# Performance work log

Hardware: AMD Instinct MI355X
Metric: run time of the kernel (lower is better)

Reference implementation:

```python
import jax, jax.numpy as jnp
import numpy as np

D_MODEL = 1024
NUM_HEADS = 16
D_K = D_MODEL // NUM_HEADS


def setup_inputs() -> dict:
    key = jax.random.key(0)
    ks = jax.random.split(key, 9)
    s = 1.0 / np.sqrt(D_MODEL)
    x = jax.random.normal(ks[0], (2, 2048, D_MODEL), dtype=jnp.float32)
    Wq = jax.random.uniform(ks[1], (D_MODEL, D_MODEL), jnp.float32, -s, s)
    bq = jax.random.uniform(ks[2], (D_MODEL,), jnp.float32, -s, s)
    Wk = jax.random.uniform(ks[3], (D_MODEL, D_MODEL), jnp.float32, -s, s)
    bk = jax.random.uniform(ks[4], (D_MODEL,), jnp.float32, -s, s)
    Wv = jax.random.uniform(ks[5], (D_MODEL, D_MODEL), jnp.float32, -s, s)
    bv = jax.random.uniform(ks[6], (D_MODEL,), jnp.float32, -s, s)
    Wo = jax.random.uniform(ks[7], (D_MODEL, D_MODEL), jnp.float32, -s, s)
    bo = jax.random.uniform(ks[8], (D_MODEL,), jnp.float32, -s, s)
    return {"x": x, "Wq": Wq, "bq": bq, "Wk": Wk, "bk": bk,
            "Wv": Wv, "bv": bv, "Wo": Wo, "bo": bo}


def reference(x, Wq, bq, Wk, bk, Wv, bv, Wo, bo):
    B, S, _ = x.shape
    # projections (torch Linear: x @ W.T + b; here W stored as [in, out])
    q = (x @ Wq + bq).reshape(B, S, NUM_HEADS, D_K).transpose(0, 2, 1, 3)
    k = (x @ Wk + bk).reshape(B, S, NUM_HEADS, D_K).transpose(0, 2, 1, 3)
    v = (x @ Wv + bv).reshape(B, S, NUM_HEADS, D_K).transpose(0, 2, 1, 3)
    scores = jnp.einsum('bhqd,bhkd->bhqk', q, k) / jnp.sqrt(jnp.float32(D_K))
    attn = jax.nn.softmax(scores, axis=-1)
    out = jnp.einsum('bhqk,bhkd->bhqd', attn, v)  # [B,H,S,Dk]
    out = out.transpose(0, 2, 1, 3).reshape(B, S, D_MODEL)
    return out @ Wo + bo
```

## Files before the change

### kernel.cpp

```cpp
#include <hip/hip_runtime.h>
#include <hip/hip_bf16.h>

#define SEQ   2048
#define DM    1024
#define NH    16
#define DK    64
#define BATCH 2
#define M_TOT 4096
#define C1 0.18033688011112042f

typedef __attribute__((ext_vector_type(8))) short bf16x8;
typedef __attribute__((ext_vector_type(4))) float f32x4;
typedef unsigned short u16;

__device__ inline u16 f2b(float f) {
    union { float f; unsigned u; } x; x.f = f;
    return (u16)((x.u + 0x7FFFu + ((x.u >> 16) & 1u)) >> 16);
}

__device__ inline unsigned pk2(float a, float b) {
    __hip_bfloat162 h = __float22bfloat162_rn(make_float2(a, b));
    return *reinterpret_cast<unsigned*>(&h);
}

__device__ inline void async_cp16(const u16* g, u16* l) {
    __builtin_amdgcn_global_load_lds(
        (const __attribute__((address_space(1))) unsigned int*)g,
        (__attribute__((address_space(3))) unsigned int*)l, 16, 0, 0);
}

__global__ __launch_bounds__(256) void cast_x(
    const float4* __restrict__ x, uint2* __restrict__ xb)
{
    int gid = blockIdx.x * 256 + threadIdx.x;
    float4 v = x[gid];
    uint2 o;
    o.x = pk2(v.x, v.y); o.y = pk2(v.z, v.w);
    xb[gid] = o;
}

__global__ __launch_bounds__(256) void transpose_cast4(
    const float* __restrict__ W0, const float* __restrict__ W1,
    const float* __restrict__ W2, const float* __restrict__ W3,
    u16* __restrict__ WtBase)
{
    __shared__ float tile[32][33];
    const int t = threadIdx.x;
    const int n0 = blockIdx.x << 5, k0 = blockIdx.y << 5, z = blockIdx.z;
    const float* W = (z == 0) ? W0 : (z == 1) ? W1 : (z == 2) ? W2 : W3;
    u16* Wt = WtBase + (size_t)z * DM * DM;
    #pragma unroll
    for (int i = 0; i < 4; ++i) {
        int idx = t + (i << 8); int r = idx >> 5, c = idx & 31;
        tile[r][c] = W[(size_t)(k0 + r) * DM + n0 + c];
    }
    __syncthreads();
    #pragma unroll
    for (int i = 0; i < 4; ++i) {
        int idx = t + (i << 8); int r = idx >> 5, c = idx & 31;
        Wt[(size_t)(n0 + r) * DM + k0 + c] = f2b(tile[c][r]);
    }
}

__global__ __launch_bounds__(256) void gemm_bt(
    const u16* __restrict__ A, const u16* __restrict__ Bt, int mode,
    const float* __restrict__ bias0, const float* __restrict__ bias1,
    const float* __restrict__ bias2,
    void* __restrict__ out0, void* __restrict__ out1, void* __restrict__ out2)
{
    __shared__ u16 sh[128 * 64 * 2];
    u16* As = sh;
    u16* Bs = sh + 128 * 64;
    const int t = threadIdx.x, wid = t >> 6, lane = t & 63;
    const int lr = lane & 15, quad = lane >> 4;
    const int m0 = blockIdx.y << 7, n0 = blockIdx.x << 7;
    const int wm = (wid & 1) << 6, wn = (wid >> 1) << 6;
    const int lrow = lane >> 3;
    const int scol = (((lane & 7) ^ lrow) << 3);
    const int c0 = ((quad ^ (lr & 7)) << 3);
    const int c1 = (((quad + 4) ^ (lr & 7)) << 3);

    f32x4 acc[4][4];
    #pragma unroll
    for (int i = 0; i < 4; ++i)
        #pragma unroll
        for (int j = 0; j < 4; ++j) acc[i][j] = (f32x4){0.f, 0.f, 0.f, 0.f};

    for (int k0 = 0; k0 < DM; k0 += 64) {
        #pragma unroll
        for (int i = 0; i < 4; ++i) {
            int rb = 32 * i + 8 * wid;
            async_cp16(A  + (size_t)(m0 + rb + lrow) * DM + k0 + scol, As + rb * 64);
            async_cp16(Bt + (size_t)(n0 + rb + lrow) * DM + k0 + scol, Bs + rb * 64);
        }
        __syncthreads();
        #pragma unroll
        for (int h = 0; h < 2; ++h) {
            const int cc = h ? c1 : c0;
            bf16x8 af[4], bfr[4];
            #pragma unroll
            for (int mt = 0; mt < 4; ++mt)
                af[mt] = *(const bf16x8*)(As + (wm + 16 * mt + lr) * 64 + cc);
            #pragma unroll
            for (int nt = 0; nt < 4; ++nt)
                bfr[nt] = *(const bf16x8*)(Bs + (wn + 16 * nt + lr) * 64 + cc);
            #pragma unroll
            for (int mt = 0; mt < 4; ++mt)
                #pragma unroll
                for (int nt = 0; nt < 4; ++nt)
                    acc[mt][nt] = __builtin_amdgcn_mfma_f32_16x16x32_bf16(
                        af[mt], bfr[nt], acc[mt][nt], 0, 0, 0);
        }
        __syncthreads();
    }

    if (mode == 1) {
        u16* wstrip = sh + wid * 1152;
        const int ngb = n0 + wn;
        const int which = ngb >> 10, nnb = ngb & 1023;
        const int h = nnb >> 6;
        const float* bp = (which == 0) ? bias0 : (which == 1) ? bias1 : bias2;
        const float sc = (which == 0) ? C1 : 1.0f;
        float bias_v[4];
        #pragma unroll
        for (int nt = 0; nt < 4; ++nt) bias_v[nt] = bp[nnb + 16 * nt + lr];

        if (which != 1) {
            u16* dst = (which == 0) ? (u16*)out0 : (u16*)out2;
            #pragma unroll
            for (int mt = 0; mt < 4; ++mt) {
                #pragma unroll
                for (int nt = 0; nt < 4; ++nt) {
                    uint2 w;
                    w.x = pk2((acc[mt][nt][0] + bias_v[nt]) * sc,
                              (acc[mt][nt][1] + bias_v[nt]) * sc);
                    w.y = pk2((acc[mt][nt][2] + bias_v[nt]) * sc,
                              (acc[mt][nt][3] + bias_v[nt]) * sc);
                    *(uint2*)(wstrip + (16 * nt + lr) * 16 + quad * 4) = w;
                }
                asm volatile("s_waitcnt lgkmcnt(0)" ::: "memory");
                #pragma unroll
                for (int half = 0; half < 2; ++half) {
                    int id = lane + 64 * half;
                    int d = id >> 1, cho = (id & 1) << 3;
                    int m = m0 + wm + 16 * mt + cho;
                    int b = m >> 11, s = m & (SEQ - 1);
                    *(uint4*)(dst + ((size_t)(b * NH + h) * DK + d) * SEQ + s) =
                        *(const uint4*)(wstrip + d * 16 + cho);
                }
                asm volatile("s_waitcnt lgkmcnt(0)" ::: "memory");
            }
        } else {
            u16* dst = (u16*)out1;
            #pragma unroll
            for (int mt = 0; mt < 4; ++mt) {
                #pragma unroll
                for (int nt = 0; nt < 4; ++nt)
                    #pragma unroll
                    for (int r = 0; r < 4; ++r)
                        wstrip[(quad * 4 + r) * 72 + 16 * nt + lr] =
                            f2b(acc[mt][nt][r] + bias_v[nt]);
                asm volatile("s_waitcnt lgkmcnt(0)" ::: "memory");
                #pragma unroll
                for (int half = 0; half < 2; ++half) {
                    int id = lane + 64 * half;
                    int mloc = id >> 3, dl = (id & 7) << 3;
                    int m = m0 + wm + 16 * mt + mloc;
                    int b = m >> 11, s = m & (SEQ - 1);
                    *(uint4*)(dst + ((size_t)(b * NH + h) * SEQ + s) * DK + dl) =
                        *(const uint4*)(wstrip + mloc * 72 + dl);
                }
                asm volatile("s_waitcnt lgkmcnt(0)" ::: "memory");
            }
        }
    } else {
        float* O = (float*)out0;
        #pragma unroll
        for (int nt = 0; nt < 4; ++nt) {
            int ng = n0 + wn + 16 * nt + lr;
            float bv_ = bias0[ng];
            #pragma unroll
            for (int mt = 0; mt < 4; ++mt) {
                int mr = m0 + wm + 16 * mt + (quad << 2);
                f32x4 v = acc[mt][nt];
                O[(size_t)mr * DM + ng]       = v.x + bv_;
                O[(size_t)(mr + 1) * DM + ng] = v.y + bv_;
                O[(size_t)(mr + 2) * DM + ng] = v.z + bv_;
                O[(size_t)(mr + 3) * DM + ng] = v.w + bv_;
            }
        }
    }
}

__global__ __launch_bounds__(256) void attn_mfma(
    const u16* __restrict__ Qt, const u16* __restrict__ K,
    const u16* __restrict__ Vt, u16* __restrict__ A)
{
    __shared__ u16 sh[20480];

    const int t = threadIdx.x, wid = t >> 6, lane = t & 63;
    const int lr = lane & 15, quad = lane >> 4;
    const int bx = blockIdx.x;
    const int xcd = bx & 7, within = bx >> 3;
    const int bh  = xcd * 4 + (within >> 5);
    const int q0  = (within & 31) << 6;

    const u16* Kb = K  + (size_t)bh * SEQ * DK;
    const u16* Vb = Vt + (size_t)bh * DK * SEQ;

    const int q = q0 + 16 * wid + lr;
    const u16* Qb = Qt + (size_t)bh * DK * SEQ + q;
    bf16x8 bQ0, bQ1;
    #pragma unroll
    for (int j = 0; j < 8; ++j) {
        bQ0[j] = (short)Qb[(size_t)(quad * 8 + j) * SEQ];
        bQ1[j] = (short)Qb[(size_t)(32 + quad * 8 + j) * SEQ];
    }

    f32x4 O[4];
    #pragma unroll
    for (int mt = 0; mt < 4; ++mt) O[mt] = (f32x4){0.f, 0.f, 0.f, 0.f};
    float l_r = 0.f;

    const int srow = t >> 3, schunk = t & 7;
    const int sslot = ((schunk ^ (srow & 7)) << 3);
    const int soff0 = srow * 64 + sslot;
    const int soff1 = (srow + 32) * 64 + sslot;
    const int c0 = ((quad ^ (lr & 7)) << 3);
    const int c1 = (((quad + 4) ^ (lr & 7)) << 3);
    const int prow = 16384 + (16 * wid + lr) * 64;

    uint4 kr0 = *(const uint4*)(Kb + (size_t)srow * DK + schunk * 8);
    uint4 kr1 = *(const uint4*)(Kb + (size_t)(srow + 32) * DK + schunk * 8);
    uint4 vr0 = *(const uint4*)(Vb + (size_t)srow * SEQ + schunk * 8);
    uint4 vr1 = *(const uint4*)(Vb + (size_t)(srow + 32) * SEQ + schunk * 8);
    *(uint4*)(sh + soff0) = kr0;
    *(uint4*)(sh + soff1) = kr1;
    *(uint4*)(sh + 8192 + soff0) = vr0;
    *(uint4*)(sh + 8192 + soff1) = vr1;
    kr0 = *(const uint4*)(Kb + (size_t)(64 + srow) * DK + schunk * 8);
    kr1 = *(const uint4*)(Kb + (size_t)(64 + srow + 32) * DK + schunk * 8);
    vr0 = *(const uint4*)(Vb + (size_t)srow * SEQ + 64 + schunk * 8);
    vr1 = *(const uint4*)(Vb + (size_t)(srow + 32) * SEQ + 64 + schunk * 8);
    __syncthreads();

    for (int it = 0; it < SEQ / 64; ++it) {
        const int kbase = (it & 1) << 12;
        const int vbase = 8192 + ((it & 1) << 12);

        f32x4 S[4];
        #pragma unroll
        for (int mt = 0; mt < 4; ++mt) {
            bf16x8 a0 = *(const bf16x8*)(sh + kbase + (16 * mt + lr) * 64 + c0);
            bf16x8 a1 = *(const bf16x8*)(sh + kbase + (16 * mt + lr) * 64 + c1);
            f32x4 s = (f32x4){0.f, 0.f, 0.f, 0.f};
            s = __builtin_amdgcn_mfma_f32_16x16x32_bf16(a0, bQ0, s, 0, 0, 0);
            s = __builtin_amdgcn_mfma_f32_16x16x32_bf16(a1, bQ1, s, 0, 0, 0);
            S[mt] = s;
        }

        #pragma unroll
        for (int mt = 0; mt < 4; ++mt) {
            float e0 = __builtin_amdgcn_exp2f(S[mt][0]);
            float e1 = __builtin_amdgcn_exp2f(S[mt][1]);
            float e2 = __builtin_amdgcn_exp2f(S[mt][2]);
            float e3 = __builtin_amdgcn_exp2f(S[mt][3]);
            l_r += (e0 + e1) + (e2 + e3);
            uint2 pk;
            pk.x = pk2(e0, e1); pk.y = pk2(e2, e3);
            int chunk = 2 * mt + (quad >> 1);
            *(uint2*)(sh + prow + ((chunk ^ (lr & 7)) << 3)
                         + ((quad & 1) << 2)) = pk;
        }
        asm volatile("s_waitcnt lgkmcnt(0)" ::: "memory");

        bf16x8 p0 = *(const bf16x8*)(sh + prow + c0);
        bf16x8 p1 = *(const bf16x8*)(sh + prow + c1);
        #pragma unroll
        for (int mt = 0; mt < 4; ++mt) {
            bf16x8 v0 = *(const bf16x8*)(sh + vbase + (16 * mt + lr) * 64 + c0);
            bf16x8 v1 = *(const bf16x8*)(sh + vbase + (16 * mt + lr) * 64 + c1);
            O[mt] = __builtin_amdgcn_mfma_f32_16x16x32_bf16(v0, p0, O[mt], 0, 0, 0);
            O[mt] = __builtin_amdgcn_mfma_f32_16x16x32_bf16(v1, p1, O[mt], 0, 0, 0);
        }

        if (it < SEQ / 64 - 1) {
            const int kn = ((it + 1) & 1) << 12;
            const int vn = 8192 + (((it + 1) & 1) << 12);
            *(uint4*)(sh + kn + soff0) = kr0;
            *(uint4*)(sh + kn + soff1) = kr1;
            *(uint4*)(sh + vn + soff0) = vr0;
            *(uint4*)(sh + vn + soff1) = vr1;
            if (it < SEQ / 64 - 2) {
                int nt2 = (it + 2) * 64;
                kr0 = *(const uint4*)(Kb + (size_t)(nt2 + srow) * DK + schunk * 8);
                kr1 = *(const uint4*)(Kb + (size_t)(nt2 + srow + 32) * DK + schunk * 8);
                vr0 = *(const uint4*)(Vb + (size_t)srow * SEQ + nt2 + schunk * 8);
                vr1 = *(const uint4*)(Vb + (size_t)(srow + 32) * SEQ + nt2 + schunk * 8);
            }
            __syncthreads();
        }
    }

    l_r += __shfl_xor(l_r, 16);
    l_r += __shfl_xor(l_r, 32);

    const int b = bh >> 4, h = bh & 15;
    float inv = 1.f / l_r;
    #pragma unroll
    for (int mt = 0; mt < 4; ++mt) {
        uint2 pk;
        pk.x = pk2(O[mt][0] * inv, O[mt][1] * inv);
        pk.y = pk2(O[mt][2] * inv, O[mt][3] * inv);
        *(uint2*)(A + (size_t)(b * SEQ + q) * DM + h * DK + 16 * mt + 4 * quad) = pk;
    }
}

extern "C" void kernel_launch(void* const* d_in, const int* in_sizes, int n_in,
                              void* d_out, int out_size, void* d_ws, size_t ws_size,
                              hipStream_t stream)
{
    const float* x  = (const float*)d_in[0];
    const float* Wq = (const float*)d_in[1];
    const float* bq = (const float*)d_in[2];
    const float* Wk = (const float*)d_in[3];
    const float* bk = (const float*)d_in[4];
    const float* Wv = (const float*)d_in[5];
    const float* bv = (const float*)d_in[6];
    const float* Wo = (const float*)d_in[7];
    const float* bo = (const float*)d_in[8];

    const size_t NE = (size_t)M_TOT * DM;
    u16* xb     = (u16*)d_ws;
    u16* wt_qkv = xb + NE;
    u16* wt_o   = wt_qkv + 3 * (size_t)DM * DM;
    u16* qt_ws  = wt_o + (size_t)DM * DM;
    u16* k_ws   = qt_ws + NE;
    u16* vt_ws  = k_ws + NE;
    u16* a_ws   = vt_ws + NE;

    cast_x<<<M_TOT * DM / 4 / 256, 256, 0, stream>>>((const float4*)x, (uint2*)xb);
    transpose_cast4<<<dim3(32, 32, 4), 256, 0, stream>>>(Wq, Wk, Wv, Wo, wt_qkv);

    gemm_bt<<<dim3(24, 32), 256, 0, stream>>>(
        xb, wt_qkv, 1, bq, bk, bv, qt_ws, k_ws, vt_ws);

    attn_mfma<<<dim3(1024), 256, 0, stream>>>(qt_ws, k_ws, vt_ws, a_ws);

    gemm_bt<<<dim3(8, 32), 256, 0, stream>>>(
        a_ws, wt_o, 0, bo, nullptr, nullptr, d_out, nullptr, nullptr);
}
```

Measured before the change: 228.4 us.

## Halve GEMM K-tile to 32 with new LDS swizzle and stage output stores through LDS

The bf16 GEMM main loop now uses a K step of 32 instead of 64, with a rotated LDS swizzle sized to the smaller tile. This cuts shared memory per block, which may allow more resident blocks, but doubles the number of barriers and loop iterations. The fp32 output-projection epilogue now writes accumulators into a padded LDS strip per wave and then stores coalesced float4 rows, replacing scattered scalar global stores.

```diff
diff --git a/kernel.cpp b/kernel.cpp
--- a/kernel.cpp
+++ b/kernel.cpp
@@ -68,17 +68,16 @@
     const float* __restrict__ bias2,
     void* __restrict__ out0, void* __restrict__ out1, void* __restrict__ out2)
 {
-    __shared__ u16 sh[128 * 64 * 2];
+    __shared__ u16 sh[9216];
     u16* As = sh;
-    u16* Bs = sh + 128 * 64;
+    u16* Bs = sh + 4096;
     const int t = threadIdx.x, wid = t >> 6, lane = t & 63;
     const int lr = lane & 15, quad = lane >> 4;
     const int m0 = blockIdx.y << 7, n0 = blockIdx.x << 7;
     const int wm = (wid & 1) << 6, wn = (wid >> 1) << 6;
-    const int lrow = lane >> 3;
-    const int scol = (((lane & 7) ^ lrow) << 3);
-    const int c0 = ((quad ^ (lr & 7)) << 3);
-    const int c1 = (((quad + 4) ^ (lr & 7)) << 3);
+    const int rowA = lane >> 2;
+    const int colA = (((lane & 3) - ((lane >> 3) & 3)) & 3) << 3;
+    const int sA = (((lr >> 1) + quad) & 3) << 3;
 
     f32x4 acc[4][4];
     #pragma unroll
@@ -86,31 +85,29 @@
         #pragma unroll
         for (int j = 0; j < 4; ++j) acc[i][j] = (f32x4){0.f, 0.f, 0.f, 0.f};
 
-    for (int k0 = 0; k0 < DM; k0 += 64) {
-        #pragma unroll
-        for (int i = 0; i < 4; ++i) {
-            int rb = 32 * i + 8 * wid;
-            async_cp16(A  + (size_t)(m0 + rb + lrow) * DM + k0 + scol, As + rb * 64);
-            async_cp16(Bt + (size_t)(n0 + rb + lrow) * DM + k0 + scol, Bs + rb * 64);
+    for (int k0 = 0; k0 < DM; k0 += 32) {
+        #pragma unroll
+        for (int i = 0; i < 2; ++i) {
+            int ch = wid * 2 + i;
+            async_cp16(A  + (size_t)(m0 + ch * 16 + rowA) * DM + k0 + colA,
+                       As + ch * 16 * 32);
+            async_cp16(Bt + (size_t)(n0 + ch * 16 + rowA) * DM + k0 + colA,
+                       Bs + ch * 16 * 32);
         }
         __syncthreads();
-        #pragma unroll
-        for (int h = 0; h < 2; ++h) {
-            const int cc = h ? c1 : c0;
-            bf16x8 af[4], bfr[4];
-            #pragma unroll
-            for (int mt = 0; mt < 4; ++mt)
-                af[mt] = *(const bf16x8*)(As + (wm + 16 * mt + lr) * 64 + cc);
+        bf16x8 af[4], bfr[4];
+        #pragma unroll
+        for (int mt = 0; mt < 4; ++mt)
+            af[mt] = *(const bf16x8*)(As + (wm + 16 * mt + lr) * 32 + sA);
+        #pragma unroll
+        for (int nt = 0; nt < 4; ++nt)
+            bfr[nt] = *(const bf16x8*)(Bs + (wn + 16 * nt + lr) * 32 + sA);
+        #pragma unroll
+        for (int mt = 0; mt < 4; ++mt)
             #pragma unroll
             for (int nt = 0; nt < 4; ++nt)
-                bfr[nt] = *(const bf16x8*)(Bs + (wn + 16 * nt + lr) * 64 + cc);
-            #pragma unroll
-            for (int mt = 0; mt < 4; ++mt)
-                #pragma unroll
-                for (int nt = 0; nt < 4; ++nt)
-                    acc[mt][nt] = __builtin_amdgcn_mfma_f32_16x16x32_bf16(
-                        af[mt], bfr[nt], acc[mt][nt], 0, 0, 0);
-        }
+                acc[mt][nt] = __builtin_amdgcn_mfma_f32_16x16x32_bf16(
+                    af[mt], bfr[nt], acc[mt][nt], 0, 0, 0);
         __syncthreads();
     }
 
@@ -175,19 +172,27 @@
         }
     } else {
         float* O = (float*)out0;
-        #pragma unroll
-        for (int nt = 0; nt < 4; ++nt) {
-            int ng = n0 + wn + 16 * nt + lr;
-            float bv_ = bias0[ng];
-            #pragma unroll
-            for (int mt = 0; mt < 4; ++mt) {
-                int mr = m0 + wm + 16 * mt + (quad << 2);
-                f32x4 v = acc[mt][nt];
-                O[(size_t)mr * DM + ng]       = v.x + bv_;
-                O[(size_t)(mr + 1) * DM + ng] = v.y + bv_;
-                O[(size_t)(mr + 2) * DM + ng] = v.z + bv_;
-                O[(size_t)(mr + 3) * DM + ng] = v.w + bv_;
+        float* strip = (float*)sh + wid * 1088;
+        float bias_v[4];
+        #pragma unroll
+        for (int nt = 0; nt < 4; ++nt) bias_v[nt] = bias0[n0 + wn + 16 * nt + lr];
+        #pragma unroll
+        for (int mt = 0; mt < 4; ++mt) {
+            #pragma unroll
+            for (int nt = 0; nt < 4; ++nt)
+                #pragma unroll
+                for (int r = 0; r < 4; ++r)
+                    strip[(quad * 4 + r) * 68 + 16 * nt + lr] =
+                        acc[mt][nt][r] + bias_v[nt];
+            asm volatile("s_waitcnt lgkmcnt(0)" ::: "memory");
+            #pragma unroll
+            for (int rr = 0; rr < 4; ++rr) {
+                int row = lane >> 2, chunk = (lane & 3) + 4 * rr;
+                float4 v = *(const float4*)(strip + row * 68 + chunk * 4);
+                *(float4*)(O + (size_t)(m0 + wm + 16 * mt + row) * DM
+                             + n0 + wn + chunk * 4) = v;
             }
+            asm volatile("s_waitcnt lgkmcnt(0)" ::: "memory");
         }
     }
 }
```

Result: faster. 216.0 us (-5.4%).
